# Kernel tuning notes

Measured on AMD Instinct MI355X. Metric: run time of the kernel, lower is better.

The kernel has to match this reference:

```python
import jax, jax.numpy as jnp
import numpy as np

N_NODES = 20000
NUM_KERNELS = 2
K_DIFF = 10  # max_diffusion_step
IN_DIM = 128
HID = 128
COMB = IN_DIM + HID  # 256
N_EDGES = 640000


def setup_inputs() -> dict:
    key = jax.random.key(0)
    ks = jax.random.split(key, 6)
    inp = jax.random.normal(ks[0], (N_NODES, IN_DIM), dtype=jnp.float32)
    hidden = jax.random.normal(ks[1], (N_NODES, HID), dtype=jnp.float32)
    edge_index = jax.random.randint(ks[2], (NUM_KERNELS, 2, N_EDGES), 0, N_NODES, dtype=jnp.int32)
    # ~row-stochastic-ish weights (avg degree 32) to keep diffusion stable
    edge_weight = jax.random.uniform(ks[3], (NUM_KERNELS, N_EDGES), dtype=jnp.float32) * (1.0 / 32.0)
    num_matrices = NUM_KERNELS * K_DIFF + 1  # 21
    W = jax.random.normal(ks[4], (num_matrices * COMB, HID), dtype=jnp.float32) * (1.0 / np.sqrt(num_matrices * COMB))
    b = jnp.zeros((HID,), dtype=jnp.float32)
    return {"input": inp, "hidden": hidden, "edge_index": edge_index,
            "edge_weight": edge_weight, "W": W, "b": b}


def _gconv(x, edge_index, edge_weight, W, b):
    # x: (N, F). Diffusion (Chebyshev) over each sparse support, concat, project.
    n = x.shape[0]
    feats = [x]  # x_0 shared across kernels
    for k in range(NUM_KERNELS):
        src = edge_index[k, 0]
        dst = edge_index[k, 1]
        w = edge_weight[k][:, None]

        def spmm(v):  # (A v)[dst] = sum_e w_e * v[src_e]
            return jax.ops.segment_sum(v[src] * w, dst, num_segments=n)

        x0, x1 = x, spmm(x)
        feats.append(x1)
        for _ in range(2, K_DIFF + 1):
            x2 = 2.0 * spmm(x1) - x0
            feats.append(x2)
            x0, x1 = x1, x2
    h = jnp.concatenate(feats, axis=1)  # (N, (NUM_KERNELS*K+1)*F)
    return h @ W + b


def reference(input, hidden, edge_index, edge_weight, W, b):
    combined = jnp.concatenate([input, hidden], axis=1)  # (N, COMB)
    r = jax.nn.sigmoid(_gconv(combined, edge_index, edge_weight, W, b))
    u = jax.nn.sigmoid(_gconv(combined, edge_index, edge_weight, W, b))
    combined2 = jnp.concatenate([input, r * hidden], axis=1)
    C = jax.nn.sigmoid(_gconv(combined2, edge_index, edge_weight, W, b))  # activation=sigmoid (default)
    output = u * hidden + (1.0 - u) * C
    return output  # output == new hidden
```

## Files before the change

### kernel.cpp

```cpp
#include <hip/hip_runtime.h>

#define NN 20000
#define NK 2
#define FC 256
#define FH 128
#define NE 640000
#define NB 21
#define ELLW 72

typedef short v8s __attribute__((ext_vector_type(8)));
typedef float v4f __attribute__((ext_vector_type(4)));
typedef unsigned int uint;
typedef uint v2u __attribute__((ext_vector_type(2)));

__device__ __forceinline__ float bf2f(unsigned short h) {
    union { uint u; float f; } v; v.u = ((uint)h) << 16; return v.f;
}
__device__ __forceinline__ unsigned short f2bf(float f) {
    union { float f; uint u; } v; v.f = f;
    uint r = v.u + 0x7FFF + ((v.u >> 16) & 1);
    return (unsigned short)(r >> 16);
}
__device__ __forceinline__ float bflo(uint v) {
    union { uint u; float f; } t; t.u = v << 16; return t.f;
}
__device__ __forceinline__ float bfhi(uint v) {
    union { uint u; float f; } t; t.u = v & 0xffff0000u; return t.f;
}


__global__ __launch_bounds__(256) void k_fill(const int* __restrict__ ei, const float* __restrict__ ew,
                                              int* __restrict__ cnt, uint* __restrict__ ell) {
    int wg = blockIdx.x;
    int xcd = wg & 7, chunk = wg >> 3;
    int k = xcd & 1, q = xcd >> 1;
    int e = chunk * 256 + threadIdx.x;
    int dst = __builtin_nontemporal_load(ei + (size_t)k * 2 * NE + NE + e);
    if (dst >= q * 5000 && dst < q * 5000 + 5000) {
        int src = __builtin_nontemporal_load(ei + (size_t)k * 2 * NE + e);
        float w = __builtin_nontemporal_load(ew + (size_t)k * NE + e);
        int slot = atomicAdd(&cnt[k * NN + dst], 1);
        if (slot < ELLW)
            ell[((size_t)k * NN + dst) * ELLW + slot] = (uint)src | ((uint)f2bf(w) << 16);
    }
}


__global__ __launch_bounds__(256) void k_comb(const float* __restrict__ in, const float* __restrict__ hid,
                                              unsigned short* __restrict__ comb) {
    int i = blockIdx.x * 256 + threadIdx.x;
    int r = i >> 6, c4 = i & 63;
    float4 v = (c4 < 32) ? ((const float4*)(in  + (size_t)r * FH))[c4]
                         : ((const float4*)(hid + (size_t)r * FH))[c4 - 32];
    ushort4 o; o.x = f2bf(v.x); o.y = f2bf(v.y); o.z = f2bf(v.z); o.w = f2bf(v.w);
    *(ushort4*)&comb[(size_t)r * FC + c4 * 4] = o;
}


__global__ __launch_bounds__(256) void k_wcvt(const float* __restrict__ W, unsigned short* __restrict__ Wt) {
    int i = blockIdx.x * 256 + threadIdx.x;
    int blk = i >> 15;
    int rem = i & 32767;
    int n = rem >> 8, kk = rem & 255;
    Wt[i] = f2bf(W[((size_t)blk * FC + kk) * FH + n]);
}


#define LDK 72

__global__ __launch_bounds__(256, 2) void k_gemm(const unsigned short* __restrict__ X,
        const unsigned short* __restrict__ Wt, unsigned short* __restrict__ outb,
        float* __restrict__ outf, int jstep) {
    __shared__ unsigned short Xs[64 * LDK];
    __shared__ unsigned short Ws[128 * LDK];
    int t = threadIdx.x;
    int w = t >> 6, l = t & 63;
    int l15 = l & 15, lg = l >> 4;
    int bm = blockIdx.x * 64;
    int blk = jstep + 10 * blockIdx.y;
    const unsigned short* Wb = Wt + (size_t)blk * FH * FC;
    v4f acc[4][2];
#pragma unroll
    for (int a = 0; a < 4; ++a)
#pragma unroll
        for (int b = 0; b < 2; ++b) acc[a][b] = (v4f){0.f, 0.f, 0.f, 0.f};

    for (int c = 0; c < 4; ++c) {
#pragma unroll
        for (int i = 0; i < 2; ++i) {
            int s = t + i * 256;
            int row = s >> 3, c8 = s & 7;
            int grow = bm + row; if (grow >= NN) grow = NN - 1;
            *(v8s*)&Xs[row * LDK + c8 * 8] = *(const v8s*)(X + (size_t)grow * FC + c * 64 + c8 * 8);
        }
#pragma unroll
        for (int i = 0; i < 4; ++i) {
            int s = t + i * 256;
            int n = s >> 3, k8 = s & 7;
            *(v8s*)&Ws[n * LDK + k8 * 8] = *(const v8s*)(Wb + (size_t)n * FC + c * 64 + k8 * 8);
        }
        __syncthreads();
#pragma unroll
        for (int ks2 = 0; ks2 < 2; ++ks2) {
            int ko = ks2 * 32 + lg * 8;
            v8s a[4], b[2];
#pragma unroll
            for (int mf = 0; mf < 4; ++mf) a[mf] = *(const v8s*)&Xs[(mf * 16 + l15) * LDK + ko];
#pragma unroll
            for (int nf = 0; nf < 2; ++nf) b[nf] = *(const v8s*)&Ws[(w * 32 + nf * 16 + l15) * LDK + ko];
#pragma unroll
            for (int mf = 0; mf < 4; ++mf)
#pragma unroll
                for (int nf = 0; nf < 2; ++nf)
                    acc[mf][nf] = __builtin_amdgcn_mfma_f32_16x16x32_bf16(a[mf], b[nf], acc[mf][nf], 0, 0, 0);
        }
        __syncthreads();
    }
    unsigned short* ob = outb ? outb + (size_t)blockIdx.y * NN * FH : (unsigned short*)0;
#pragma unroll
    for (int mf = 0; mf < 4; ++mf) {
        int grow0 = bm + mf * 16 + lg * 4;
#pragma unroll
        for (int nf = 0; nf < 2; ++nf) {
            int gcol = w * 32 + nf * 16 + l15;
            int hh = gcol >> 6, c63 = gcol & 63;
#pragma unroll
            for (int r = 0; r < 4; ++r) {
                int grow = grow0 + r;
                if (grow < NN) {
                    if (outf) outf[(size_t)grow * FH + gcol] = acc[mf][nf][r];
                    else      ob[((size_t)hh * NN + grow) * 64 + c63] = f2bf(acc[mf][nf][r]);
                }
            }
        }
    }
}


__global__ __launch_bounds__(256) void k_spmm(const int* __restrict__ cnt, const uint* __restrict__ ell,
        const v2u* __restrict__ b1, const v2u* __restrict__ b2,
        const v2u* __restrict__ y, v2u* __restrict__ outp, int mode) {
    int wg = blockIdx.x;
    int g = wg & 7, slot = wg >> 3;
    int k = g >> 2, h = (g >> 1) & 1, rh = g & 1;
    int lane = threadIdx.x & 63;
    int l15 = lane & 15, sl = lane >> 4;
    int row = (rh * 2500 + slot) * 4 + (threadIdx.x >> 6);
    int d = cnt[k * NN + row];
    if (d > ELLW) d = ELLW;
    const uint* __restrict__ er = ell + ((size_t)k * NN + row) * ELLW;
    const v2u* __restrict__ gb = b1 + (size_t)(k * 2 + h) * NN * 16;

    size_t o = ((size_t)(k * 2 + h) * NN + row) * 16 + l15;
    v2u yv = (v2u){0, 0}, bv = (v2u){0, 0};
    if (mode != 2) yv = __builtin_nontemporal_load(y + o);
    if (mode != 0) bv = b2[o];

    float a0 = 0.f, a1 = 0.f, a2 = 0.f, a3 = 0.f;

    uint mc[4];
#pragma unroll
    for (int u = 0; u < 4; ++u) {
        int idx = u * 4 + sl;
        mc[u] = (idx < d) ? er[idx] : 0u;
    }
    for (int e0 = 0; e0 < d; e0 += 16) {
        uint mn[4];
        int e1 = e0 + 16;
        if (e1 + 16 <= d) {
#pragma unroll
            for (int u = 0; u < 4; ++u) mn[u] = er[e1 + u * 4 + sl];
        } else {
#pragma unroll
            for (int u = 0; u < 4; ++u) {
                int idx = e1 + u * 4 + sl;
                mn[u] = (idx < d) ? er[idx] : 0u;
            }
        }
#pragma unroll
        for (int u = 0; u < 4; ++u) {
            uint m = mc[u];
            float w = bfhi(m);
            v2u vv = gb[(uint)((m & 0xffffu) * 16 + l15)];
            a0 += w * bflo(vv.x); a1 += w * bfhi(vv.x);
            a2 += w * bflo(vv.y); a3 += w * bfhi(vv.y);
        }
#pragma unroll
        for (int u = 0; u < 4; ++u) mc[u] = mn[u];
    }

    a0 += __shfl_xor(a0, 16); a1 += __shfl_xor(a1, 16);
    a2 += __shfl_xor(a2, 16); a3 += __shfl_xor(a3, 16);
    a0 += __shfl_xor(a0, 32); a1 += __shfl_xor(a1, 32);
    a2 += __shfl_xor(a2, 32); a3 += __shfl_xor(a3, 32);

    if (lane < 16) {
        float r0, r1, r2, r3;
        if (mode == 0) {
            r0 = bflo(yv.x) + 2.f * a0; r1 = bfhi(yv.x) + 2.f * a1;
            r2 = bflo(yv.y) + 2.f * a2; r3 = bfhi(yv.y) + 2.f * a3;
        } else if (mode == 1) {
            r0 = bflo(yv.x) + 2.f * a0 - bflo(bv.x); r1 = bfhi(yv.x) + 2.f * a1 - bfhi(bv.x);
            r2 = bflo(yv.y) + 2.f * a2 - bflo(bv.y); r3 = bfhi(yv.y) + 2.f * a3 - bfhi(bv.y);
        } else {
            r0 = a0 - bflo(bv.x); r1 = a1 - bfhi(bv.x);
            r2 = a2 - bflo(bv.y); r3 = a3 - bfhi(bv.y);
        }
        v2u res;
        res.x = (uint)f2bf(r0) | ((uint)f2bf(r1) << 16);
        res.y = (uint)f2bf(r2) | ((uint)f2bf(r3) << 16);
        outp[o] = res;
    }
}


__global__ __launch_bounds__(256) void k_act(const float* __restrict__ S0, const unsigned short* __restrict__ Sk,
        const float* __restrict__ bvec, const float* __restrict__ hid,
        float* __restrict__ rbuf, unsigned short* __restrict__ comb) {
    int i = blockIdx.x * 256 + threadIdx.x;
    int r = i >> 7, c = i & 127;
    int h = c >> 6, c63 = c & 63;
    float s = S0[i] + bf2f(Sk[((size_t)h * NN + r) * 64 + c63])
                    + bf2f(Sk[((size_t)(2 + h) * NN + r) * 64 + c63]) + bvec[c];
    float u = 1.f / (1.f + __expf(-s));
    rbuf[i] = u;
    comb[(size_t)r * FC + FH + c] = f2bf(u * hid[i]);
}

__global__ __launch_bounds__(256) void k_final(const float* __restrict__ S0, const unsigned short* __restrict__ Sk,
        const float* __restrict__ bvec, const float* __restrict__ hid,
        const float* __restrict__ rbuf, float* __restrict__ out) {
    int i = blockIdx.x * 256 + threadIdx.x;
    int r = i >> 7, c = i & 127;
    int h = c >> 6, c63 = c & 63;
    float s = S0[i] + bf2f(Sk[((size_t)h * NN + r) * 64 + c63])
                    + bf2f(Sk[((size_t)(2 + h) * NN + r) * 64 + c63]) + bvec[c];
    float C = 1.f / (1.f + __expf(-s));
    float u = rbuf[i];
    out[i] = u * hid[i] + (1.f - u) * C;
}


extern "C" void kernel_launch(void* const* d_in, const int* in_sizes, int n_in,
                              void* d_out, int out_size, void* d_ws, size_t ws_size,
                              hipStream_t stream) {
    const float* inp = (const float*)d_in[0];
    const float* hid = (const float*)d_in[1];
    const int*   ei  = (const int*)d_in[2];
    const float* ew  = (const float*)d_in[3];
    const float* W   = (const float*)d_in[4];
    const float* bv  = (const float*)d_in[5];
    float* out = (float*)d_out;

    char* base = (char*)d_ws;
    size_t off = 0;
    auto carve = [&](size_t bytes) -> char* {
        char* q = base + off;
        off += (bytes + 255) & ~(size_t)255;
        return q;
    };
    int*            cnt  = (int*)carve((size_t)2 * NN * 4);
    uint*           ell  = (uint*)carve(((size_t)2 * NN * ELLW + 128) * 4);
    unsigned short* comb = (unsigned short*)carve((size_t)NN * FC * 2);
    unsigned short* Wt   = (unsigned short*)carve((size_t)NB * FH * FC * 2);
    unsigned short* ytmp = (unsigned short*)carve((size_t)2 * NN * FH * 2);
    unsigned short* Bs0  = (unsigned short*)carve((size_t)2 * NN * FH * 2);
    unsigned short* Bs1  = (unsigned short*)carve((size_t)2 * NN * FH * 2);
    unsigned short* Bs2  = (unsigned short*)carve((size_t)2 * NN * FH * 2);
    float*          Sacc = (float*)carve((size_t)NN * FH * 4);
    float*          rbuf = (float*)carve((size_t)NN * FH * 4);
    unsigned short* Bsl[3] = {Bs0, Bs1, Bs2};

    hipMemsetAsync(cnt, 0, (size_t)2 * NN * 4, stream);
    k_fill<<<20000, 256, 0, stream>>>(ei, ew, cnt, ell);
    k_comb<<<5000, 256, 0, stream>>>(inp, hid, comb);
    k_wcvt<<<2688, 256, 0, stream>>>(W, Wt);

    auto gemm = [&](int j, unsigned short* ob, float* of, int gy) {
        k_gemm<<<dim3(313, gy), 256, 0, stream>>>(comb, Wt, ob, of, j);
    };
    auto spmm = [&](unsigned short* b1, unsigned short* b2, unsigned short* y,
                    unsigned short* o, int mode) {
        k_spmm<<<20000, 256, 0, stream>>>(cnt, ell, (const v2u*)b1, (const v2u*)b2,
                                          (const v2u*)y, (v2u*)o, mode);
    };

    auto gconv = [&]() -> unsigned short* {
        gemm(0, nullptr, Sacc, 1);
        gemm(10, Bsl[0], nullptr, 2);
        gemm(9, ytmp, nullptr, 2);
        spmm(Bsl[0], nullptr, ytmp, Bsl[1], 0);
        int cur = 1, prev = 0;
        for (int j = 8; j >= 1; --j) {
            int nxt = 3 - cur - prev;
            gemm(j, ytmp, nullptr, 2);
            spmm(Bsl[cur], Bsl[prev], ytmp, Bsl[nxt], 1);
            prev = cur; cur = nxt;
        }
        int fr = 3 - cur - prev;
        spmm(Bsl[cur], Bsl[prev], nullptr, Bsl[fr], 2);
        return Bsl[fr];
    };

    unsigned short* S1 = gconv();
    k_act<<<10000, 256, 0, stream>>>(Sacc, S1, bv, hid, rbuf, comb);
    unsigned short* S2 = gconv();
    k_final<<<10000, 256, 0, stream>>>(Sacc, S2, bv, hid, rbuf, out);
}
```

Before: 1.104 ms.

## Widen SpMM gathers to 16 bytes and batch GEMM steps in pairs

The SpMM now gathers 16-byte vectors per lane, with 8 lanes per row and 8 edge slots in parallel. It drops the register prefetch and instead zero-fills a wider ELL buffer (96 slots) so the tail loads need no bounds checks. The GEMM launches now compute two diffusion steps per launch into two y buffers, halving the number of GEMM launches. The costs are an extra memset of the larger ELL array, more padded edges to process, and the loss of the next-chunk prefetch.

Result: no change. 1.117 ms (+1.2%).

```diff
diff --git a/kernel.cpp b/kernel.cpp
--- a/kernel.cpp
+++ b/kernel.cpp
@@ -6,12 +6,12 @@
 #define FH 128
 #define NE 640000
 #define NB 21
-#define ELLW 72
+#define ELLW 96
 
 typedef short v8s __attribute__((ext_vector_type(8)));
 typedef float v4f __attribute__((ext_vector_type(4)));
 typedef unsigned int uint;
-typedef uint v2u __attribute__((ext_vector_type(2)));
+typedef uint v4u __attribute__((ext_vector_type(4)));
 
 __device__ __forceinline__ float bf2f(unsigned short h) {
     union { uint u; float f; } v; v.u = ((uint)h) << 16; return v.f;
@@ -69,15 +69,17 @@
 #define LDK 72
 
 __global__ __launch_bounds__(256, 2) void k_gemm(const unsigned short* __restrict__ X,
-        const unsigned short* __restrict__ Wt, unsigned short* __restrict__ outb,
-        float* __restrict__ outf, int jstep) {
+        const unsigned short* __restrict__ Wt, unsigned short* __restrict__ obA,
+        unsigned short* __restrict__ obB, float* __restrict__ outf, int jstep) {
     __shared__ unsigned short Xs[64 * LDK];
     __shared__ unsigned short Ws[128 * LDK];
     int t = threadIdx.x;
     int w = t >> 6, l = t & 63;
     int l15 = l & 15, lg = l >> 4;
     int bm = blockIdx.x * 64;
-    int blk = jstep + 10 * blockIdx.y;
+    int by = blockIdx.y;
+    int sup = by & 1, dj = by >> 1;
+    int blk = outf ? 0 : ((jstep - dj) + 10 * sup);
     const unsigned short* Wb = Wt + (size_t)blk * FH * FC;
     v4f acc[4][2];
 #pragma unroll
@@ -116,7 +118,8 @@
         }
         __syncthreads();
     }
-    unsigned short* ob = outb ? outb + (size_t)blockIdx.y * NN * FH : (unsigned short*)0;
+    unsigned short* ob = (dj ? obB : obA);
+    if (ob) ob += (size_t)sup * NN * FH;
 #pragma unroll
     for (int mf = 0; mf < 4; ++mf) {
         int grow0 = bm + mf * 16 + lg * 4;
@@ -138,77 +141,69 @@
 
 
 __global__ __launch_bounds__(256) void k_spmm(const int* __restrict__ cnt, const uint* __restrict__ ell,
-        const v2u* __restrict__ b1, const v2u* __restrict__ b2,
-        const v2u* __restrict__ y, v2u* __restrict__ outp, int mode) {
+        const v4u* __restrict__ b1, const v4u* __restrict__ b2,
+        const v4u* __restrict__ y, v4u* __restrict__ outp, int mode) {
     int wg = blockIdx.x;
     int g = wg & 7, slot = wg >> 3;
     int k = g >> 2, h = (g >> 1) & 1, rh = g & 1;
     int lane = threadIdx.x & 63;
-    int l15 = lane & 15, sl = lane >> 4;
+    int l7 = lane & 7, sl = lane >> 3;
     int row = (rh * 2500 + slot) * 4 + (threadIdx.x >> 6);
     int d = cnt[k * NN + row];
     if (d > ELLW) d = ELLW;
     const uint* __restrict__ er = ell + ((size_t)k * NN + row) * ELLW;
-    const v2u* __restrict__ gb = b1 + (size_t)(k * 2 + h) * NN * 16;
-
-    size_t o = ((size_t)(k * 2 + h) * NN + row) * 16 + l15;
-    v2u yv = (v2u){0, 0}, bv = (v2u){0, 0};
+    const v4u* __restrict__ gb = b1 + (size_t)(k * 2 + h) * NN * 8;
+
+    size_t o = ((size_t)(k * 2 + h) * NN + row) * 8 + l7;
+    v4u yv = (v4u){0, 0, 0, 0}, bv = (v4u){0, 0, 0, 0};
     if (mode != 2) yv = __builtin_nontemporal_load(y + o);
     if (mode != 0) bv = b2[o];
 
-    float a0 = 0.f, a1 = 0.f, a2 = 0.f, a3 = 0.f;
-
-    uint mc[4];
-#pragma unroll
-    for (int u = 0; u < 4; ++u) {
-        int idx = u * 4 + sl;
-        mc[u] = (idx < d) ? er[idx] : 0u;
-    }
-    for (int e0 = 0; e0 < d; e0 += 16) {
-        uint mn[4];
-        int e1 = e0 + 16;
-        if (e1 + 16 <= d) {
-#pragma unroll
-            for (int u = 0; u < 4; ++u) mn[u] = er[e1 + u * 4 + sl];
-        } else {
-#pragma unroll
-            for (int u = 0; u < 4; ++u) {
-                int idx = e1 + u * 4 + sl;
-                mn[u] = (idx < d) ? er[idx] : 0u;
-            }
-        }
+    float a0 = 0.f, a1 = 0.f, a2 = 0.f, a3 = 0.f, a4 = 0.f, a5 = 0.f, a6 = 0.f, a7 = 0.f;
+
+    for (int e0 = 0; e0 < d; e0 += 32) {
 #pragma unroll
         for (int u = 0; u < 4; ++u) {
-            uint m = mc[u];
+            uint m = __builtin_nontemporal_load(er + e0 + u * 8 + sl);
             float w = bfhi(m);
-            v2u vv = gb[(uint)((m & 0xffffu) * 16 + l15)];
+            v4u vv = gb[(uint)((m & 0xffffu) * 8 + l7)];
             a0 += w * bflo(vv.x); a1 += w * bfhi(vv.x);
             a2 += w * bflo(vv.y); a3 += w * bfhi(vv.y);
-        }
-#pragma unroll
-        for (int u = 0; u < 4; ++u) mc[u] = mn[u];
-    }
-
-    a0 += __shfl_xor(a0, 16); a1 += __shfl_xor(a1, 16);
-    a2 += __shfl_xor(a2, 16); a3 += __shfl_xor(a3, 16);
-    a0 += __shfl_xor(a0, 32); a1 += __shfl_xor(a1, 32);
-    a2 += __shfl_xor(a2, 32); a3 += __shfl_xor(a3, 32);
-
-    if (lane < 16) {
-        float r0, r1, r2, r3;
+            a4 += w * bflo(vv.z); a5 += w * bfhi(vv.z);
+            a6 += w * bflo(vv.w); a7 += w * bfhi(vv.w);
+        }
+    }
+
+    a0 += __shfl_xor(a0, 8);  a1 += __shfl_xor(a1, 8);  a2 += __shfl_xor(a2, 8);  a3 += __shfl_xor(a3, 8);
+    a4 += __shfl_xor(a4, 8);  a5 += __shfl_xor(a5, 8);  a6 += __shfl_xor(a6, 8);  a7 += __shfl_xor(a7, 8);
+    a0 += __shfl_xor(a0, 16); a1 += __shfl_xor(a1, 16); a2 += __shfl_xor(a2, 16); a3 += __shfl_xor(a3, 16);
+    a4 += __shfl_xor(a4, 16); a5 += __shfl_xor(a5, 16); a6 += __shfl_xor(a6, 16); a7 += __shfl_xor(a7, 16);
+    a0 += __shfl_xor(a0, 32); a1 += __shfl_xor(a1, 32); a2 += __shfl_xor(a2, 32); a3 += __shfl_xor(a3, 32);
+    a4 += __shfl_xor(a4, 32); a5 += __shfl_xor(a5, 32); a6 += __shfl_xor(a6, 32); a7 += __shfl_xor(a7, 32);
+
+    if (lane < 8) {
+        float r0, r1, r2, r3, r4, r5, r6, r7;
         if (mode == 0) {
             r0 = bflo(yv.x) + 2.f * a0; r1 = bfhi(yv.x) + 2.f * a1;
             r2 = bflo(yv.y) + 2.f * a2; r3 = bfhi(yv.y) + 2.f * a3;
+            r4 = bflo(yv.z) + 2.f * a4; r5 = bfhi(yv.z) + 2.f * a5;
+            r6 = bflo(yv.w) + 2.f * a6; r7 = bfhi(yv.w) + 2.f * a7;
         } else if (mode == 1) {
             r0 = bflo(yv.x) + 2.f * a0 - bflo(bv.x); r1 = bfhi(yv.x) + 2.f * a1 - bfhi(bv.x);
             r2 = bflo(yv.y) + 2.f * a2 - bflo(bv.y); r3 = bfhi(yv.y) + 2.f * a3 - bfhi(bv.y);
+            r4 = bflo(yv.z) + 2.f * a4 - bflo(bv.z); r5 = bfhi(yv.z) + 2.f * a5 - bfhi(bv.z);
+            r6 = bflo(yv.w) + 2.f * a6 - bflo(bv.w); r7 = bfhi(yv.w) + 2.f * a7 - bfhi(bv.w);
         } else {
             r0 = a0 - bflo(bv.x); r1 = a1 - bfhi(bv.x);
             r2 = a2 - bflo(bv.y); r3 = a3 - bfhi(bv.y);
-        }
-        v2u res;
+            r4 = a4 - bflo(bv.z); r5 = a5 - bfhi(bv.z);
+            r6 = a6 - bflo(bv.w); r7 = a7 - bfhi(bv.w);
+        }
+        v4u res;
         res.x = (uint)f2bf(r0) | ((uint)f2bf(r1) << 16);
         res.y = (uint)f2bf(r2) | ((uint)f2bf(r3) << 16);
+        res.z = (uint)f2bf(r4) | ((uint)f2bf(r5) << 16);
+        res.w = (uint)f2bf(r6) | ((uint)f2bf(r7) << 16);
         outp[o] = res;
     }
 }
@@ -260,10 +255,11 @@
         return q;
     };
     int*            cnt  = (int*)carve((size_t)2 * NN * 4);
-    uint*           ell  = (uint*)carve(((size_t)2 * NN * ELLW + 128) * 4);
+    uint*           ell  = (uint*)carve((size_t)2 * NN * ELLW * 4);
     unsigned short* comb = (unsigned short*)carve((size_t)NN * FC * 2);
     unsigned short* Wt   = (unsigned short*)carve((size_t)NB * FH * FC * 2);
-    unsigned short* ytmp = (unsigned short*)carve((size_t)2 * NN * FH * 2);
+    unsigned short* ytA  = (unsigned short*)carve((size_t)2 * NN * FH * 2);
+    unsigned short* ytB  = (unsigned short*)carve((size_t)2 * NN * FH * 2);
     unsigned short* Bs0  = (unsigned short*)carve((size_t)2 * NN * FH * 2);
     unsigned short* Bs1  = (unsigned short*)carve((size_t)2 * NN * FH * 2);
     unsigned short* Bs2  = (unsigned short*)carve((size_t)2 * NN * FH * 2);
@@ -272,29 +268,35 @@
     unsigned short* Bsl[3] = {Bs0, Bs1, Bs2};
 
     hipMemsetAsync(cnt, 0, (size_t)2 * NN * 4, stream);
+    hipMemsetAsync(ell, 0, (size_t)2 * NN * ELLW * 4, stream);
     k_fill<<<20000, 256, 0, stream>>>(ei, ew, cnt, ell);
     k_comb<<<5000, 256, 0, stream>>>(inp, hid, comb);
     k_wcvt<<<2688, 256, 0, stream>>>(W, Wt);
 
-    auto gemm = [&](int j, unsigned short* ob, float* of, int gy) {
-        k_gemm<<<dim3(313, gy), 256, 0, stream>>>(comb, Wt, ob, of, j);
+    auto gemmId = [&]() {
+        k_gemm<<<dim3(313, 1), 256, 0, stream>>>(comb, Wt, nullptr, nullptr, Sacc, 0);
+    };
+    auto gemmPair = [&](int j, unsigned short* oA, unsigned short* oB) {
+        k_gemm<<<dim3(313, 4), 256, 0, stream>>>(comb, Wt, oA, oB, nullptr, j);
     };
     auto spmm = [&](unsigned short* b1, unsigned short* b2, unsigned short* y,
                     unsigned short* o, int mode) {
-        k_spmm<<<20000, 256, 0, stream>>>(cnt, ell, (const v2u*)b1, (const v2u*)b2,
-                                          (const v2u*)y, (v2u*)o, mode);
+        k_spmm<<<20000, 256, 0, stream>>>(cnt, ell, (const v4u*)b1, (const v4u*)b2,
+                                          (const v4u*)y, (v4u*)o, mode);
     };
 
     auto gconv = [&]() -> unsigned short* {
-        gemm(0, nullptr, Sacc, 1);
-        gemm(10, Bsl[0], nullptr, 2);
-        gemm(9, ytmp, nullptr, 2);
-        spmm(Bsl[0], nullptr, ytmp, Bsl[1], 0);
+        gemmId();
+        gemmPair(10, Bsl[0], ytA);
+        spmm(Bsl[0], nullptr, ytA, Bsl[1], 0);
         int cur = 1, prev = 0;
-        for (int j = 8; j >= 1; --j) {
+        for (int jp = 8; jp >= 2; jp -= 2) {
+            gemmPair(jp, ytA, ytB);
             int nxt = 3 - cur - prev;
-            gemm(j, ytmp, nullptr, 2);
-            spmm(Bsl[cur], Bsl[prev], ytmp, Bsl[nxt], 1);
+            spmm(Bsl[cur], Bsl[prev], ytA, Bsl[nxt], 1);
+            prev = cur; cur = nxt;
+            nxt = 3 - cur - prev;
+            spmm(Bsl[cur], Bsl[prev], ytB, Bsl[nxt], 1);
             prev = cur; cur = nxt;
         }
         int fr = 3 - cur - prev;
```
